# Optimization experiments

Measured on AMD Instinct MI355X. Metric: run time of the kernel, lower is better.

Reference implementation:

```python
import jax, jax.numpy as jnp
import numpy as np

B, T, H, K = 4, 4096, 2048, 4
FREQ_BINS = H // 2  # int(hidden_size * freq_ratio) with freq_ratio=0.5


def setup_inputs() -> dict:
    key = jax.random.key(0)
    k1, k2 = jax.random.split(key, 2)
    x = jax.random.normal(k1, (B, T, H), dtype=jnp.float32)
    # kernel_weights = ones + 0.02*randn, shape (n_kernels, freq_bins)
    kernel_weights = 1.0 + 0.02 * jax.random.normal(k2, (K, FREQ_BINS), dtype=jnp.float32)
    thresholds = jnp.full((K,), 0.1, dtype=jnp.float32)
    # blend_proj: Linear(n_kernels, 1, bias=False), weight (1, K) init to 1/K
    blend_w = jnp.full((1, K), 1.0 / K, dtype=jnp.float32)
    return {"x": x, "kernel_weights": kernel_weights, "thresholds": thresholds, "blend_w": blend_w}


def reference(x, kernel_weights, thresholds, blend_w):
    # energy per token: L2 norm over hidden dim -> (B, T)
    energy = jnp.linalg.norm(x, axis=-1)
    # threshold-gated routing: (B, T, K) binary gate (non-differentiable)
    gate = (energy[..., None] > jnp.abs(thresholds)[None, None, :]).astype(jnp.float32)
    # rfft over hidden dim, keep real part of first freq_bins bins
    fb = kernel_weights.shape[1]
    x_fft_real = jnp.fft.rfft(x.astype(jnp.float32), axis=-1).real[..., :fb]  # (B, T, fb)
    # per-kernel spectral projection
    scaled = jnp.einsum('btf,kf->btk', x_fft_real, kernel_weights)  # (B, T, K)
    activated = scaled * gate
    # blend to scalar map + tanh -> (B, T, 1)
    mod = jnp.tanh(jnp.einsum('btk,ok->bto', activated, blend_w))
    return mod.astype(x.dtype)
```

## Files before the change

kernel.cpp:

```cpp
#include <hip/hip_runtime.h>
#include <math.h>

#define HDIM 2048
#define FB   1024
#define NK   4
#define NTOK 16384

typedef float f32x4 __attribute__((ext_vector_type(4)));

__global__ __launch_bounds__(256) void build_eff(const float* __restrict__ w,
                                                 float* __restrict__ e) {
    int gid = blockIdx.x * 256 + threadIdx.x;
    int oid = gid >> 4;
    int sub = gid & 15;
    int k = oid >> 11;
    int n = oid & 2047;
    const float* wk = w + k * FB;

    const float inv = 1.0f / 2048.0f;
    int step = (n << 4) & 2047;
    int p = (n * sub) & 2047;
    float acc = 0.0f;
#pragma unroll 8
    for (int j = 0; j < 64; ++j) {
        int f = (j << 4) + sub;
        acc = fmaf(wk[f], __builtin_amdgcn_cosf((float)p * inv), acc);
        p = (p + step) & 2047;
    }
    acc += __shfl_xor(acc, 1);
    acc += __shfl_xor(acc, 2);
    acc += __shfl_xor(acc, 4);
    acc += __shfl_xor(acc, 8);
    if (sub == 0) e[oid] = acc;
}

__device__ __forceinline__ float finish_tok(float en, const float* a,
                                            const float* th, const float* bl) {
    float energy = sqrtf(en);
    float z = 0.0f;
#pragma unroll
    for (int k = 0; k < NK; ++k)
        if (energy > th[k]) z = fmaf(bl[k], a[k], z);
    return tanhf(z);
}

__global__ __launch_bounds__(256, 4) void spectral_main(
    const float* __restrict__ x,
    const float* __restrict__ e,
    const float* __restrict__ thr,
    const float* __restrict__ blend,
    float* __restrict__ out) {
    __shared__ f32x4 els[NK * HDIM / 4];

    int tid = threadIdx.x;
    int wave = tid >> 6;
    int lane = tid & 63;
    int tok0 = blockIdx.x * 16 + wave * 4;
    const f32x4* xr = (const f32x4*)x + (size_t)tok0 * (HDIM / 4);

    f32x4 xv0[4], xv1[4];
#pragma unroll
    for (int t = 0; t < 4; ++t) {
        xv0[t] = __builtin_nontemporal_load(&xr[t * 512 + 0 * 64 + lane]);
        xv1[t] = __builtin_nontemporal_load(&xr[t * 512 + 1 * 64 + lane]);
    }

    const f32x4* eg = (const f32x4*)e;
#pragma unroll
    for (int i = 0; i < 8; ++i) els[i * 256 + tid] = eg[i * 256 + tid];

    float th[NK], bl[NK];
#pragma unroll
    for (int k = 0; k < NK; ++k) { th[k] = fabsf(thr[k]); bl[k] = blend[k]; }

    __syncthreads();

    float en[4] = {0.f, 0.f, 0.f, 0.f};
    float ac[4][NK] = {};

#pragma unroll
    for (int c = 0; c < 8; ++c) {
        int idx = c * 64 + lane;
        f32x4 ev[NK];
#pragma unroll
        for (int k = 0; k < NK; ++k) ev[k] = els[k * 512 + idx];
        f32x4 xv[4];
        if (c == 0) {
#pragma unroll
            for (int t = 0; t < 4; ++t) xv[t] = xv0[t];
        } else if (c == 1) {
#pragma unroll
            for (int t = 0; t < 4; ++t) xv[t] = xv1[t];
        } else {
#pragma unroll
            for (int t = 0; t < 4; ++t)
                xv[t] = __builtin_nontemporal_load(&xr[t * 512 + idx]);
        }
#pragma unroll
        for (int t = 0; t < 4; ++t) {
            f32x4 v = xv[t];
            en[t] = fmaf(v.x, v.x, fmaf(v.y, v.y, fmaf(v.z, v.z, fmaf(v.w, v.w, en[t]))));
#pragma unroll
            for (int k = 0; k < NK; ++k) {
                f32x4 w4 = ev[k];
                ac[t][k] = fmaf(v.x, w4.x, fmaf(v.y, w4.y,
                           fmaf(v.z, w4.z, fmaf(v.w, w4.w, ac[t][k]))));
            }
        }
    }

#pragma unroll
    for (int s = 1; s < 64; s <<= 1) {
#pragma unroll
        for (int t = 0; t < 4; ++t) {
            en[t] += __shfl_xor(en[t], s);
#pragma unroll
            for (int k = 0; k < NK; ++k) ac[t][k] += __shfl_xor(ac[t][k], s);
        }
    }

    if (lane == 0) {
        f32x4 o;
        o.x = finish_tok(en[0], ac[0], th, bl);
        o.y = finish_tok(en[1], ac[1], th, bl);
        o.z = finish_tok(en[2], ac[2], th, bl);
        o.w = finish_tok(en[3], ac[3], th, bl);
        *(f32x4*)(out + tok0) = o;
    }
}

extern "C" void kernel_launch(void* const* d_in, const int* in_sizes, int n_in,
                              void* d_out, int out_size, void* d_ws, size_t ws_size,
                              hipStream_t stream) {
    const float* x     = (const float*)d_in[0];
    const float* w     = (const float*)d_in[1];
    const float* thr   = (const float*)d_in[2];
    const float* blend = (const float*)d_in[3];
    float* out = (float*)d_out;
    float* e   = (float*)d_ws;

    build_eff<<<512, 256, 0, stream>>>(w, e);
    spectral_main<<<NTOK / 16, 256, 0, stream>>>(x, e, thr, blend, out);
}
```

Before: 32.95 us.

## Fuse weight-transform and main pass into one cooperative kernel with grid sync

Merges the effective-weight build (cosine transform of kernel weights) and the main token reduction into one cooperative kernel of 1024 blocks. Each block first issues prefetch loads for three chunks of x, then computes its share of the transform, then waits at a grid-wide sync. This removes one kernel launch and overlaps x loads with the transform, at the cost of a grid barrier and extra registers held across it. The old two-kernel path is kept as a fallback if the cooperative launch fails.

```diff
diff --git a/kernel.cpp b/kernel.cpp
--- a/kernel.cpp
+++ b/kernel.cpp
@@ -1,12 +1,136 @@
 #include <hip/hip_runtime.h>
+#include <hip/hip_cooperative_groups.h>
 #include <math.h>
+
+namespace cg = cooperative_groups;
 
 #define HDIM 2048
 #define FB   1024
 #define NK   4
 #define NTOK 16384
+#define NBLK 1024
+#define PF   3
 
 typedef float f32x4 __attribute__((ext_vector_type(4)));
+
+__device__ __forceinline__ float finish_tok(float en, const float* a,
+                                            const float* th, const float* bl) {
+    float energy = sqrtf(en);
+    float z = 0.0f;
+#pragma unroll
+    for (int k = 0; k < NK; ++k)
+        if (energy > th[k]) z = fmaf(bl[k], a[k], z);
+    return tanhf(z);
+}
+
+__global__ __launch_bounds__(256, 4) void spectral_fused(
+    const float* __restrict__ x,
+    const float* __restrict__ w,
+    const float* __restrict__ thr,
+    const float* __restrict__ blend,
+    float* __restrict__ out,
+    float* __restrict__ e) {
+    __shared__ f32x4 els[NK * HDIM / 4];
+
+    int tid = threadIdx.x;
+    int wave = tid >> 6;
+    int lane = tid & 63;
+    int tok0 = blockIdx.x * 16 + wave * 4;
+    const f32x4* xr = (const f32x4*)x + (size_t)tok0 * (HDIM / 4);
+
+    f32x4 pf[PF][4];
+#pragma unroll
+    for (int c = 0; c < PF; ++c)
+#pragma unroll
+        for (int t = 0; t < 4; ++t)
+            pf[c][t] = __builtin_nontemporal_load(&xr[t * 512 + c * 64 + lane]);
+
+    {
+        int gid = blockIdx.x * 256 + tid;
+        int oid = gid >> 5;
+        int sub = gid & 31;
+        int k = oid >> 11;
+        int n = oid & 2047;
+        const float* wk = w + k * FB;
+        const float inv = 1.0f / 2048.0f;
+        int step = (n << 5) & 2047;
+        int p = (n * sub) & 2047;
+        float acc = 0.0f;
+#pragma unroll 8
+        for (int j = 0; j < 32; ++j) {
+            acc = fmaf(wk[(j << 5) + sub], __builtin_amdgcn_cosf((float)p * inv), acc);
+            p = (p + step) & 2047;
+        }
+        acc += __shfl_xor(acc, 1);
+        acc += __shfl_xor(acc, 2);
+        acc += __shfl_xor(acc, 4);
+        acc += __shfl_xor(acc, 8);
+        acc += __shfl_xor(acc, 16);
+        if (sub == 0) e[oid] = acc;
+    }
+
+    cg::this_grid().sync();
+
+    const f32x4* eg = (const f32x4*)e;
+#pragma unroll
+    for (int i = 0; i < 8; ++i) els[i * 256 + tid] = eg[i * 256 + tid];
+
+    float th[NK], bl[NK];
+#pragma unroll
+    for (int k = 0; k < NK; ++k) { th[k] = fabsf(thr[k]); bl[k] = blend[k]; }
+
+    __syncthreads();
+
+    float en[4] = {0.f, 0.f, 0.f, 0.f};
+    float ac[4][NK] = {};
+
+#pragma unroll
+    for (int c = 0; c < 8; ++c) {
+        int idx = c * 64 + lane;
+        f32x4 ev[NK];
+#pragma unroll
+        for (int k = 0; k < NK; ++k) ev[k] = els[k * 512 + idx];
+        f32x4 xv[4];
+        if (c < PF) {
+#pragma unroll
+            for (int t = 0; t < 4; ++t) xv[t] = pf[c][t];
+        } else {
+#pragma unroll
+            for (int t = 0; t < 4; ++t)
+                xv[t] = __builtin_nontemporal_load(&xr[t * 512 + idx]);
+        }
+#pragma unroll
+        for (int t = 0; t < 4; ++t) {
+            f32x4 v = xv[t];
+            en[t] = fmaf(v.x, v.x, fmaf(v.y, v.y, fmaf(v.z, v.z, fmaf(v.w, v.w, en[t]))));
+#pragma unroll
+            for (int k = 0; k < NK; ++k) {
+                f32x4 w4 = ev[k];
+                ac[t][k] = fmaf(v.x, w4.x, fmaf(v.y, w4.y,
+                           fmaf(v.z, w4.z, fmaf(v.w, w4.w, ac[t][k]))));
+            }
+        }
+    }
+
+#pragma unroll
+    for (int s = 1; s < 64; s <<= 1) {
+#pragma unroll
+        for (int t = 0; t < 4; ++t) {
+            en[t] += __shfl_xor(en[t], s);
+#pragma unroll
+            for (int k = 0; k < NK; ++k) ac[t][k] += __shfl_xor(ac[t][k], s);
+        }
+    }
+
+    if (lane == 0) {
+        f32x4 o;
+        o.x = finish_tok(en[0], ac[0], th, bl);
+        o.y = finish_tok(en[1], ac[1], th, bl);
+        o.z = finish_tok(en[2], ac[2], th, bl);
+        o.w = finish_tok(en[3], ac[3], th, bl);
+        *(f32x4*)(out + tok0) = o;
+    }
+}
 
 __global__ __launch_bounds__(256) void build_eff(const float* __restrict__ w,
                                                  float* __restrict__ e) {
@@ -16,15 +140,13 @@
     int k = oid >> 11;
     int n = oid & 2047;
     const float* wk = w + k * FB;
-
     const float inv = 1.0f / 2048.0f;
     int step = (n << 4) & 2047;
     int p = (n * sub) & 2047;
     float acc = 0.0f;
 #pragma unroll 8
     for (int j = 0; j < 64; ++j) {
-        int f = (j << 4) + sub;
-        acc = fmaf(wk[f], __builtin_amdgcn_cosf((float)p * inv), acc);
+        acc = fmaf(wk[(j << 4) + sub], __builtin_amdgcn_cosf((float)p * inv), acc);
         p = (p + step) & 2047;
     }
     acc += __shfl_xor(acc, 1);
@@ -32,16 +154,6 @@
     acc += __shfl_xor(acc, 4);
     acc += __shfl_xor(acc, 8);
     if (sub == 0) e[oid] = acc;
-}
-
-__device__ __forceinline__ float finish_tok(float en, const float* a,
-                                            const float* th, const float* bl) {
-    float energy = sqrtf(en);
-    float z = 0.0f;
-#pragma unroll
-    for (int k = 0; k < NK; ++k)
-        if (energy > th[k]) z = fmaf(bl[k], a[k], z);
-    return tanhf(z);
 }
 
 __global__ __launch_bounds__(256, 4) void spectral_main(
@@ -51,54 +163,31 @@
     const float* __restrict__ blend,
     float* __restrict__ out) {
     __shared__ f32x4 els[NK * HDIM / 4];
-
     int tid = threadIdx.x;
     int wave = tid >> 6;
     int lane = tid & 63;
     int tok0 = blockIdx.x * 16 + wave * 4;
     const f32x4* xr = (const f32x4*)x + (size_t)tok0 * (HDIM / 4);
 
-    f32x4 xv0[4], xv1[4];
-#pragma unroll
-    for (int t = 0; t < 4; ++t) {
-        xv0[t] = __builtin_nontemporal_load(&xr[t * 512 + 0 * 64 + lane]);
-        xv1[t] = __builtin_nontemporal_load(&xr[t * 512 + 1 * 64 + lane]);
-    }
-
     const f32x4* eg = (const f32x4*)e;
 #pragma unroll
     for (int i = 0; i < 8; ++i) els[i * 256 + tid] = eg[i * 256 + tid];
-
     float th[NK], bl[NK];
 #pragma unroll
     for (int k = 0; k < NK; ++k) { th[k] = fabsf(thr[k]); bl[k] = blend[k]; }
-
     __syncthreads();
 
     float en[4] = {0.f, 0.f, 0.f, 0.f};
     float ac[4][NK] = {};
-
 #pragma unroll
     for (int c = 0; c < 8; ++c) {
         int idx = c * 64 + lane;
         f32x4 ev[NK];
 #pragma unroll
         for (int k = 0; k < NK; ++k) ev[k] = els[k * 512 + idx];
-        f32x4 xv[4];
-        if (c == 0) {
-#pragma unroll
-            for (int t = 0; t < 4; ++t) xv[t] = xv0[t];
-        } else if (c == 1) {
-#pragma unroll
-            for (int t = 0; t < 4; ++t) xv[t] = xv1[t];
-        } else {
-#pragma unroll
-            for (int t = 0; t < 4; ++t)
-                xv[t] = __builtin_nontemporal_load(&xr[t * 512 + idx]);
-        }
-#pragma unroll
-        for (int t = 0; t < 4; ++t) {
-            f32x4 v = xv[t];
+#pragma unroll
+        for (int t = 0; t < 4; ++t) {
+            f32x4 v = __builtin_nontemporal_load(&xr[t * 512 + idx]);
             en[t] = fmaf(v.x, v.x, fmaf(v.y, v.y, fmaf(v.z, v.z, fmaf(v.w, v.w, en[t]))));
 #pragma unroll
             for (int k = 0; k < NK; ++k) {
@@ -108,7 +197,6 @@
             }
         }
     }
-
 #pragma unroll
     for (int s = 1; s < 64; s <<= 1) {
 #pragma unroll
@@ -118,7 +206,6 @@
             for (int k = 0; k < NK; ++k) ac[t][k] += __shfl_xor(ac[t][k], s);
         }
     }
-
     if (lane == 0) {
         f32x4 o;
         o.x = finish_tok(en[0], ac[0], th, bl);
@@ -139,6 +226,13 @@
     float* out = (float*)d_out;
     float* e   = (float*)d_ws;
 
-    build_eff<<<512, 256, 0, stream>>>(w, e);
-    spectral_main<<<NTOK / 16, 256, 0, stream>>>(x, e, thr, blend, out);
-}
+    void* args[] = {(void*)&x, (void*)&w, (void*)&thr, (void*)&blend,
+                    (void*)&out, (void*)&e};
+    hipError_t err = hipLaunchCooperativeKernel((const void*)spectral_fused,
+                                                dim3(NBLK), dim3(256),
+                                                args, 0, stream);
+    if (err != hipSuccess) {
+        build_eff<<<512, 256, 0, stream>>>(w, e);
+        spectral_main<<<NTOK / 16, 256, 0, stream>>>(x, e, thr, blend, out);
+    }
+}
```

Result: slower. 126.9 us (+285.0%).
